# Kernel tuning notes

Measured on AMD Instinct MI355X. Metric: run time of the kernel, lower is better.

## Reference

```python
import jax, jax.numpy as jnp
import numpy as np

D_MODEL = 1024
NUM_HEADS = 16
D_K = D_MODEL // NUM_HEADS          # 64
D_ROPE = int(D_K * 0.5)             # 32
ROPE_BASE = 10000.0


def _rope(x):
    # x: [L, B, H, D_K]; rotate first D_ROPE features, pass the rest through.
    L = x.shape[0]
    d = D_ROPE
    theta = 1.0 / (ROPE_BASE ** (jnp.arange(0, d, 2, dtype=jnp.float32) / d))  # [d/2]
    idx_theta = jnp.arange(L, dtype=jnp.float32)[:, None] * theta[None, :]     # [L, d/2]
    idx_theta2 = jnp.concatenate([idx_theta, idx_theta], axis=-1)              # [L, d]
    cos = jnp.cos(idx_theta2)[:, None, None, :].astype(x.dtype)
    sin = jnp.sin(idx_theta2)[:, None, None, :].astype(x.dtype)
    x_rope, x_pass = x[..., :d], x[..., d:]
    neg_half = jnp.concatenate([-x_rope[..., d // 2:], x_rope[..., :d // 2]], axis=-1)
    x_rope = x_rope * cos + neg_half * sin
    return jnp.concatenate([x_rope, x_pass], axis=-1)


def setup_inputs() -> dict:
    key = jax.random.key(0)
    k1, k2 = jax.random.split(key)
    L, B = 2048, 2
    x = jax.random.normal(k1, (L, B, D_MODEL), dtype=jnp.float32)
    # xavier_uniform-like init for in_proj_weight [3*d_model, d_model]
    limit = float(np.sqrt(6.0 / (3 * D_MODEL + D_MODEL)))
    in_proj_weight = jax.random.uniform(k2, (3 * D_MODEL, D_MODEL),
                                        minval=-limit, maxval=limit, dtype=jnp.float32)
    return {"x": x, "in_proj_weight": in_proj_weight}


def reference(x, in_proj_weight):
    L, B, _ = x.shape
    # fused QKV projection: [L, B, 3*d_model]
    qkv = jnp.einsum('ed,lbd->lbe', in_proj_weight, x)
    # NOTE: faithful to original quirk — reshape to per-head blocks of 3*d_k,
    # then chunk along last dim.
    qkv = qkv.reshape(L, B, NUM_HEADS, 3 * D_K)
    q, k, v = qkv[..., :D_K], qkv[..., D_K:2 * D_K], qkv[..., 2 * D_K:]
    q = _rope(q)
    k = _rope(k)
    # [L,B,H,dk] -> [H,B,L,dk]
    q, k, v = (jnp.swapaxes(t, 0, 2) for t in (q, k, v))
    scale = 1.0 / jnp.sqrt(jnp.asarray(D_K, dtype=x.dtype))
    scores = jnp.einsum('hbqd,hbkd->hbqk', q, k) * scale      # [H,B,L,L]
    attn = jax.nn.softmax(scores, axis=-1)
    out = jnp.einsum('hbqk,hbkd->hbqd', attn, v)              # [H,B,L,dk]
    out = jnp.transpose(out, (1, 2, 0, 3)).reshape(B, L, D_MODEL)
    return jnp.swapaxes(out, 0, 1)                            # [L,B,D] (batch_first falsy)
```

## Files before the change

### kernel.cpp

```cpp
#include <hip/hip_runtime.h>
#include <cstdint>
#include <cstddef>

#define L_SEQ 2048
#define BATCH 2
#define DM 1024
#define NH 16
#define DK 64
#define QKV_N 3072
#define HEAD_STRIDE 192
#define NX (4096 * 1024)
#define NW (3072 * 1024)

typedef short short8_t __attribute__((ext_vector_type(8)));
typedef short short4_t __attribute__((ext_vector_type(4)));
typedef float f32x4 __attribute__((ext_vector_type(4)));

#define MFMA16(a, b, c) __builtin_amdgcn_mfma_f32_16x16x32_bf16(a, b, c, 0, 0, 0)

static __device__ __forceinline__ short f2b(float f) {
  union { float f; unsigned u; } v; v.f = f;
  unsigned r = v.u + 0x7FFFu + ((v.u >> 16) & 1u);
  return (short)(r >> 16);
}

static __device__ __forceinline__ void async_copy16(const unsigned short* g,
                                                    unsigned short* l) {
  __builtin_amdgcn_global_load_lds(
      (const __attribute__((address_space(1))) unsigned int*)g,
      (__attribute__((address_space(3))) unsigned int*)l, 16, 0, 0);
}

__global__ __launch_bounds__(256) void cast_kernel(
    const float* __restrict__ X, const float* __restrict__ W,
    unsigned short* __restrict__ dst) {
  const int e = (blockIdx.x * 256 + threadIdx.x) * 8;
  const float* src = (e < NX) ? &X[e] : &W[e - NX];
  const float4 v0 = *(const float4*)src;
  const float4 v1 = *(const float4*)(src + 4);
  short8_t s;
  s[0] = f2b(v0.x); s[1] = f2b(v0.y); s[2] = f2b(v0.z); s[3] = f2b(v0.w);
  s[4] = f2b(v1.x); s[5] = f2b(v1.y); s[6] = f2b(v1.z); s[7] = f2b(v1.w);
  *(short8_t*)&dst[e] = s;
}

__global__ __launch_bounds__(256) void qkv_gemm_bf16(
    const unsigned short* __restrict__ Xb, const unsigned short* __restrict__ Wb,
    unsigned short* __restrict__ qkvb) {
  __shared__ __align__(16) unsigned short As[128 * 32];
  __shared__ __align__(16) unsigned short Bs[128 * 32];
  const int t = threadIdx.x;
  const int w = t >> 6;
  const int lane = t & 63;
  const int L16 = lane & 15;
  const int quad = lane >> 4;
  const int m0 = blockIdx.y * 128;
  const int n0 = blockIdx.x * 128;
  const int wm = w & 1;
  const int wn = w >> 1;

  const int c0 = w * 128 + lane;
  const int c1 = c0 + 64;
  const unsigned short* gA0 = Xb + (size_t)(m0 + (c0 >> 2)) * 1024 + (c0 & 3) * 8;
  const unsigned short* gA1 = Xb + (size_t)(m0 + (c1 >> 2)) * 1024 + (c1 & 3) * 8;
  const unsigned short* gB0 = Wb + (size_t)(n0 + (c0 >> 2)) * 1024 + (c0 & 3) * 8;
  const unsigned short* gB1 = Wb + (size_t)(n0 + (c1 >> 2)) * 1024 + (c1 & 3) * 8;
  unsigned short* lA0 = &As[(w * 128) * 8];
  unsigned short* lA1 = &As[(w * 128 + 64) * 8];
  unsigned short* lB0 = &Bs[(w * 128) * 8];
  unsigned short* lB1 = &Bs[(w * 128 + 64) * 8];

  f32x4 acc[4][4];
#pragma unroll
  for (int i = 0; i < 4; ++i)
#pragma unroll
    for (int j = 0; j < 4; ++j) acc[i][j] = (f32x4){0.f, 0.f, 0.f, 0.f};

  for (int k0 = 0; k0 < 1024; k0 += 32) {
    async_copy16(gA0 + k0, lA0);
    async_copy16(gA1 + k0, lA1);
    async_copy16(gB0 + k0, lB0);
    async_copy16(gB1 + k0, lB1);
    __syncthreads();

    short8_t af[4], bfr[4];
#pragma unroll
    for (int mt = 0; mt < 4; ++mt)
      af[mt] = *(const short8_t*)&As[(wm * 64 + mt * 16 + L16) * 32 + quad * 8];
#pragma unroll
    for (int nt = 0; nt < 4; ++nt)
      bfr[nt] = *(const short8_t*)&Bs[(wn * 64 + nt * 16 + L16) * 32 + quad * 8];
#pragma unroll
    for (int mt = 0; mt < 4; ++mt)
#pragma unroll
      for (int nt = 0; nt < 4; ++nt)
        acc[mt][nt] = MFMA16(af[mt], bfr[nt], acc[mt][nt]);
    __syncthreads();
  }

  const int nbase = n0 + wn * 64 + L16;
  const int chunk = (n0 >> 6) + wn;
  const int type = chunk % 3;
  if (type == 2) {
#pragma unroll
    for (int mt = 0; mt < 4; ++mt) {
      const int mbase = m0 + wm * 64 + mt * 16 + quad * 4;
#pragma unroll
      for (int reg = 0; reg < 4; ++reg) {
        const size_t r = (size_t)(mbase + reg) * QKV_N + nbase;
        qkvb[r]      = (unsigned short)f2b(acc[mt][0][reg]);
        qkvb[r + 16] = (unsigned short)f2b(acc[mt][1][reg]);
        qkvb[r + 32] = (unsigned short)f2b(acc[mt][2][reg]);
        qkvb[r + 48] = (unsigned short)f2b(acc[mt][3][reg]);
      }
    }
  } else {
    const float qs = (type == 0) ? 0.125f : 1.0f;
    const float theta = exp2f(-(float)L16 * 0.8304820237218405f);
#pragma unroll
    for (int mt = 0; mt < 4; ++mt) {
      const int mbase = m0 + wm * 64 + mt * 16 + quad * 4;
      const int lb = mbase >> 1;
      float sv[2], cv[2];
      sincosf((float)lb * theta, &sv[0], &cv[0]);
      sincosf((float)(lb + 1) * theta, &sv[1], &cv[1]);
#pragma unroll
      for (int reg = 0; reg < 4; ++reg) {
        const int li = reg >> 1;
        const float v0 = acc[mt][0][reg], v1 = acc[mt][1][reg];
        const float r0 = v0 * cv[li] - v1 * sv[li];
        const float r1 = v1 * cv[li] + v0 * sv[li];
        const size_t r = (size_t)(mbase + reg) * QKV_N + nbase;
        qkvb[r]      = (unsigned short)f2b(r0 * qs);
        qkvb[r + 16] = (unsigned short)f2b(r1 * qs);
        qkvb[r + 32] = (unsigned short)f2b(acc[mt][2][reg] * qs);
        qkvb[r + 48] = (unsigned short)f2b(acc[mt][3][reg] * qs);
      }
    }
  }
}

__global__ __launch_bounds__(256) void attn_mfma_kernel(
    const unsigned short* __restrict__ qkvb, float* __restrict__ out) {
  __shared__ __align__(16) unsigned short Qs[128][72];
  __shared__ __align__(16) unsigned short Ks[64][72];
  __shared__ __align__(16) unsigned short Vt[64][72];
  __shared__ __align__(16) unsigned short Pw[4][32][72];

  const int t = threadIdx.x;
  const int w = t >> 6;
  const int lane = t & 63;
  const int L16 = lane & 15;
  const int quad = lane >> 4;
  const int l0 = blockIdx.x * 128;
  const int b = blockIdx.y & 1;
  const int h = blockIdx.y >> 1;
  const int hoff = h * HEAD_STRIDE;

#pragma unroll
  for (int it = 0; it < 4; ++it) {
    const int c = t + 256 * it;
    const int row = c >> 3;
    const int col = (c & 7) * 8;
    *(short8_t*)&Qs[row][col] =
        *(const short8_t*)&qkvb[((size_t)((l0 + row) * 2 + b)) * QKV_N + hoff + col];
  }
  __syncthreads();

  const short8_t aq00 = *(const short8_t*)&Qs[w * 32 + L16][quad * 8];
  const short8_t aq01 = *(const short8_t*)&Qs[w * 32 + L16][32 + quad * 8];
  const short8_t aq10 = *(const short8_t*)&Qs[w * 32 + 16 + L16][quad * 8];
  const short8_t aq11 = *(const short8_t*)&Qs[w * 32 + 16 + L16][32 + quad * 8];

  f32x4 oc[2][4];
  float l_part[2][4];
#pragma unroll
  for (int mt = 0; mt < 2; ++mt)
#pragma unroll
    for (int r = 0; r < 4; ++r) {
      l_part[mt][r] = 0.f;
      oc[mt][r] = (f32x4){0.f, 0.f, 0.f, 0.f};
    }

  const int krow0 = t >> 3, kcol0 = (t & 7) * 8;
  const int krow1 = (t + 256) >> 3, kcol1 = (t & 7) * 8;
  const int vr4 = (t >> 4) * 4;
  const int vc4 = (t & 15) * 4;
  const int cgbase = vr4 >> 3;
  const int joff = vr4 & 7;
  short8_t rk0, rk1;
  short4_t rv[4];

#define LOAD_TILE(KT)                                                         \
  {                                                                           \
    const int j0 = (KT) * 64;                                                 \
    rk0 = *(const short8_t*)&qkvb[((size_t)((j0 + krow0) * 2 + b)) * QKV_N +  \
                                  hoff + 64 + kcol0];                         \
    rk1 = *(const short8_t*)&qkvb[((size_t)((j0 + krow1) * 2 + b)) * QKV_N +  \
                                  hoff + 64 + kcol1];                         \
    _Pragma("unroll") for (int r = 0; r < 4; ++r)                             \
        rv[r] = *(const short4_t*)&qkvb[((size_t)((j0 + vr4 + r) * 2 + b)) *  \
                                        QKV_N + hoff + 128 + vc4];            \
  }

  LOAD_TILE(0)

  for (int kt = 0; kt < 32; ++kt) {
    __syncthreads();
    *(short8_t*)&Ks[krow0][kcol0] = rk0;
    *(short8_t*)&Ks[krow1][kcol1] = rk1;
    {
      short4_t s[4];
      s[0] = (short4_t){rv[0][0], rv[1][0], rv[2][0], rv[3][0]};
      s[1] = (short4_t){rv[0][1], rv[1][1], rv[2][1], rv[3][1]};
      s[2] = (short4_t){rv[0][2], rv[1][2], rv[2][2], rv[3][2]};
      s[3] = (short4_t){rv[0][3], rv[1][3], rv[2][3], rv[3][3]};
#pragma unroll
      for (int i = 0; i < 4; ++i) {
        const int d = vc4 + i;
        const int cg = (cgbase + ((d >> 2) & 7)) & 7;
        *(short4_t*)&Vt[d][cg * 8 + joff] = s[i];
      }
    }
    if (kt + 1 < 32) LOAD_TILE(kt + 1)
    __syncthreads();

    f32x4 sc[2][4];
#pragma unroll
    for (int mt = 0; mt < 2; ++mt)
#pragma unroll
      for (int nt = 0; nt < 4; ++nt) sc[mt][nt] = (f32x4){0.f, 0.f, 0.f, 0.f};
#pragma unroll
    for (int nt = 0; nt < 4; ++nt) {
      const short8_t b0 = *(const short8_t*)&Ks[nt * 16 + L16][quad * 8];
      const short8_t b1 = *(const short8_t*)&Ks[nt * 16 + L16][32 + quad * 8];
      sc[0][nt] = MFMA16(aq00, b0, sc[0][nt]);
      sc[0][nt] = MFMA16(aq01, b1, sc[0][nt]);
      sc[1][nt] = MFMA16(aq10, b0, sc[1][nt]);
      sc[1][nt] = MFMA16(aq11, b1, sc[1][nt]);
    }

#pragma unroll
    for (int mt = 0; mt < 2; ++mt) {
#pragma unroll
      for (int reg = 0; reg < 4; ++reg) {
        const int prow = mt * 16 + quad * 4 + reg;
#pragma unroll
        for (int nt = 0; nt < 4; ++nt) {
          const float p = __expf(sc[mt][nt][reg]);
          l_part[mt][reg] += p;
          Pw[w][prow][nt * 16 + L16] = (unsigned short)f2b(p);
        }
      }
    }

    const short8_t ap00 = *(const short8_t*)&Pw[w][L16][quad * 8];
    const short8_t ap01 = *(const short8_t*)&Pw[w][L16][32 + quad * 8];
    const short8_t ap10 = *(const short8_t*)&Pw[w][16 + L16][quad * 8];
    const short8_t ap11 = *(const short8_t*)&Pw[w][16 + L16][32 + quad * 8];
#pragma unroll
    for (int dt = 0; dt < 4; ++dt) {
      const int d = dt * 16 + L16;
      const int sh = (d >> 2) & 7;
      const short8_t bv0 = *(const short8_t*)&Vt[d][((quad + sh) & 7) * 8];
      const short8_t bv1 = *(const short8_t*)&Vt[d][((quad + 4 + sh) & 7) * 8];
      oc[0][dt] = MFMA16(ap00, bv0, oc[0][dt]);
      oc[0][dt] = MFMA16(ap01, bv1, oc[0][dt]);
      oc[1][dt] = MFMA16(ap10, bv0, oc[1][dt]);
      oc[1][dt] = MFMA16(ap11, bv1, oc[1][dt]);
    }
  }

#pragma unroll
  for (int mt = 0; mt < 2; ++mt) {
#pragma unroll
    for (int reg = 0; reg < 4; ++reg) {
      float l = l_part[mt][reg];
      l += __shfl_xor(l, 1);
      l += __shfl_xor(l, 2);
      l += __shfl_xor(l, 4);
      l += __shfl_xor(l, 8);
      const float inv = 1.f / l;
      const int qrow = l0 + w * 32 + mt * 16 + quad * 4 + reg;
      const size_t rbase = ((size_t)(qrow * 2 + b)) * DM + h * DK + L16;
#pragma unroll
      for (int dt = 0; dt < 4; ++dt) {
        out[rbase + dt * 16] = oc[mt][dt][reg] * inv;
      }
    }
  }
}

extern "C" void kernel_launch(void* const* d_in, const int* in_sizes, int n_in,
                              void* d_out, int out_size, void* d_ws,
                              size_t ws_size, hipStream_t stream) {
  const float* x = (const float*)d_in[0];
  const float* w = (const float*)d_in[1];
  float* out = (float*)d_out;
  unsigned short* bf = (unsigned short*)d_ws;
  unsigned short* Xb = bf;
  unsigned short* Wb = bf + NX;
  unsigned short* qkvb =
      (unsigned short*)((char*)d_ws + (16u << 20));

  cast_kernel<<<(NX + NW) / (256 * 8), 256, 0, stream>>>(x, w, bf);
  qkv_gemm_bf16<<<dim3(QKV_N / 128, (L_SEQ * BATCH) / 128), 256, 0, stream>>>(
      Xb, Wb, qkvb);
  attn_mfma_kernel<<<dim3(L_SEQ / 128, NH * BATCH), 256, 0, stream>>>(qkvb, out);
}
```

Baseline: 193.8 us.

## Compute transposed scores so P stays in registers, drop K/Q/P LDS staging

The attention kernel now computes S^T (K as the A operand, Q as B), so each lane's accumulator holds four consecutive keys for one query. Those probabilities can feed a 16x16x16 bf16 MFMA directly as the B operand, which removes the per-warp P round trip through LDS. Q and K fragments are loaded straight from global memory into registers instead of being staged in shared memory. V is double-buffered in LDS so one barrier per tile suffices, the output is written with float4 stores, and occupancy is hinted via launch bounds. The cost is more global K traffic, since each warp reloads K rather than sharing it, and twice as many smaller MFMA instructions for the PV product.

```diff
diff --git a/kernel.cpp b/kernel.cpp
--- a/kernel.cpp
+++ b/kernel.cpp
@@ -16,7 +16,8 @@
 typedef short short4_t __attribute__((ext_vector_type(4)));
 typedef float f32x4 __attribute__((ext_vector_type(4)));
 
-#define MFMA16(a, b, c) __builtin_amdgcn_mfma_f32_16x16x32_bf16(a, b, c, 0, 0, 0)
+#define MFMA32(a, b, c) __builtin_amdgcn_mfma_f32_16x16x32_bf16(a, b, c, 0, 0, 0)
+#define MFMA16(a, b, c) __builtin_amdgcn_mfma_f32_16x16x16bf16_1k(a, b, c, 0, 0, 0)
 
 static __device__ __forceinline__ short f2b(float f) {
   union { float f; unsigned u; } v; v.f = f;
@@ -94,7 +95,7 @@
     for (int mt = 0; mt < 4; ++mt)
 #pragma unroll
       for (int nt = 0; nt < 4; ++nt)
-        acc[mt][nt] = MFMA16(af[mt], bfr[nt], acc[mt][nt]);
+        acc[mt][nt] = MFMA32(af[mt], bfr[nt], acc[mt][nt]);
     __syncthreads();
   }
 
@@ -140,12 +141,9 @@
   }
 }
 
-__global__ __launch_bounds__(256) void attn_mfma_kernel(
+__global__ __launch_bounds__(256, 4) void attn_mfma_kernel(
     const unsigned short* __restrict__ qkvb, float* __restrict__ out) {
-  __shared__ __align__(16) unsigned short Qs[128][72];
-  __shared__ __align__(16) unsigned short Ks[64][72];
-  __shared__ __align__(16) unsigned short Vt[64][72];
-  __shared__ __align__(16) unsigned short Pw[4][32][72];
+  __shared__ __align__(16) unsigned short Vt[2][64][72];
 
   const int t = threadIdx.x;
   const int w = t >> 6;
@@ -157,58 +155,40 @@
   const int h = blockIdx.y >> 1;
   const int hoff = h * HEAD_STRIDE;
 
-#pragma unroll
-  for (int it = 0; it < 4; ++it) {
-    const int c = t + 256 * it;
-    const int row = c >> 3;
-    const int col = (c & 7) * 8;
-    *(short8_t*)&Qs[row][col] =
-        *(const short8_t*)&qkvb[((size_t)((l0 + row) * 2 + b)) * QKV_N + hoff + col];
-  }
-  __syncthreads();
-
-  const short8_t aq00 = *(const short8_t*)&Qs[w * 32 + L16][quad * 8];
-  const short8_t aq01 = *(const short8_t*)&Qs[w * 32 + L16][32 + quad * 8];
-  const short8_t aq10 = *(const short8_t*)&Qs[w * 32 + 16 + L16][quad * 8];
-  const short8_t aq11 = *(const short8_t*)&Qs[w * 32 + 16 + L16][32 + quad * 8];
+  short8_t bq[2][2];
+#pragma unroll
+  for (int mt = 0; mt < 2; ++mt)
+#pragma unroll
+    for (int kc = 0; kc < 2; ++kc)
+      bq[mt][kc] = *(const short8_t*)
+          &qkvb[((size_t)((l0 + w * 32 + mt * 16 + L16) * 2 + b)) * QKV_N +
+                hoff + kc * 32 + quad * 8];
 
   f32x4 oc[2][4];
-  float l_part[2][4];
+  float l_part[2] = {0.f, 0.f};
 #pragma unroll
   for (int mt = 0; mt < 2; ++mt)
 #pragma unroll
-    for (int r = 0; r < 4; ++r) {
-      l_part[mt][r] = 0.f;
-      oc[mt][r] = (f32x4){0.f, 0.f, 0.f, 0.f};
-    }
-
-  const int krow0 = t >> 3, kcol0 = (t & 7) * 8;
-  const int krow1 = (t + 256) >> 3, kcol1 = (t & 7) * 8;
+    for (int dt = 0; dt < 4; ++dt) oc[mt][dt] = (f32x4){0.f, 0.f, 0.f, 0.f};
+
   const int vr4 = (t >> 4) * 4;
   const int vc4 = (t & 15) * 4;
   const int cgbase = vr4 >> 3;
   const int joff = vr4 & 7;
-  short8_t rk0, rk1;
   short4_t rv[4];
 
-#define LOAD_TILE(KT)                                                         \
+#define LOAD_V(KT)                                                            \
   {                                                                           \
     const int j0 = (KT) * 64;                                                 \
-    rk0 = *(const short8_t*)&qkvb[((size_t)((j0 + krow0) * 2 + b)) * QKV_N +  \
-                                  hoff + 64 + kcol0];                         \
-    rk1 = *(const short8_t*)&qkvb[((size_t)((j0 + krow1) * 2 + b)) * QKV_N +  \
-                                  hoff + 64 + kcol1];                         \
     _Pragma("unroll") for (int r = 0; r < 4; ++r)                             \
         rv[r] = *(const short4_t*)&qkvb[((size_t)((j0 + vr4 + r) * 2 + b)) *  \
                                         QKV_N + hoff + 128 + vc4];            \
   }
 
-  LOAD_TILE(0)
+  LOAD_V(0)
 
   for (int kt = 0; kt < 32; ++kt) {
-    __syncthreads();
-    *(short8_t*)&Ks[krow0][kcol0] = rk0;
-    *(short8_t*)&Ks[krow1][kcol1] = rk1;
+    const int buf = kt & 1;
     {
       short4_t s[4];
       s[0] = (short4_t){rv[0][0], rv[1][0], rv[2][0], rv[3][0]};
@@ -219,12 +199,14 @@
       for (int i = 0; i < 4; ++i) {
         const int d = vc4 + i;
         const int cg = (cgbase + ((d >> 2) & 7)) & 7;
-        *(short4_t*)&Vt[d][cg * 8 + joff] = s[i];
-      }
-    }
-    if (kt + 1 < 32) LOAD_TILE(kt + 1)
+        *(short4_t*)&Vt[buf][d][cg * 8 + joff] = s[i];
+      }
+    }
+    if (kt + 1 < 32) LOAD_V(kt + 1)
     __syncthreads();
 
+    const int j0 = kt * 64;
+
     f32x4 sc[2][4];
 #pragma unroll
     for (int mt = 0; mt < 2; ++mt)
@@ -232,61 +214,56 @@
       for (int nt = 0; nt < 4; ++nt) sc[mt][nt] = (f32x4){0.f, 0.f, 0.f, 0.f};
 #pragma unroll
     for (int nt = 0; nt < 4; ++nt) {
-      const short8_t b0 = *(const short8_t*)&Ks[nt * 16 + L16][quad * 8];
-      const short8_t b1 = *(const short8_t*)&Ks[nt * 16 + L16][32 + quad * 8];
-      sc[0][nt] = MFMA16(aq00, b0, sc[0][nt]);
-      sc[0][nt] = MFMA16(aq01, b1, sc[0][nt]);
-      sc[1][nt] = MFMA16(aq10, b0, sc[1][nt]);
-      sc[1][nt] = MFMA16(aq11, b1, sc[1][nt]);
-    }
-
+      const size_t krow = (size_t)((j0 + nt * 16 + L16) * 2 + b) * QKV_N + hoff + 64;
+      const short8_t ak0 = *(const short8_t*)&qkvb[krow + quad * 8];
+      const short8_t ak1 = *(const short8_t*)&qkvb[krow + 32 + quad * 8];
+      sc[0][nt] = MFMA32(ak0, bq[0][0], sc[0][nt]);
+      sc[0][nt] = MFMA32(ak1, bq[0][1], sc[0][nt]);
+      sc[1][nt] = MFMA32(ak0, bq[1][0], sc[1][nt]);
+      sc[1][nt] = MFMA32(ak1, bq[1][1], sc[1][nt]);
+    }
+
+    short4_t pf[2][4];
 #pragma unroll
     for (int mt = 0; mt < 2; ++mt) {
 #pragma unroll
-      for (int reg = 0; reg < 4; ++reg) {
-        const int prow = mt * 16 + quad * 4 + reg;
-#pragma unroll
-        for (int nt = 0; nt < 4; ++nt) {
-          const float p = __expf(sc[mt][nt][reg]);
-          l_part[mt][reg] += p;
-          Pw[w][prow][nt * 16 + L16] = (unsigned short)f2b(p);
-        }
-      }
-    }
-
-    const short8_t ap00 = *(const short8_t*)&Pw[w][L16][quad * 8];
-    const short8_t ap01 = *(const short8_t*)&Pw[w][L16][32 + quad * 8];
-    const short8_t ap10 = *(const short8_t*)&Pw[w][16 + L16][quad * 8];
-    const short8_t ap11 = *(const short8_t*)&Pw[w][16 + L16][32 + quad * 8];
+      for (int nt = 0; nt < 4; ++nt) {
+        float p0 = __expf(sc[mt][nt][0]);
+        float p1 = __expf(sc[mt][nt][1]);
+        float p2 = __expf(sc[mt][nt][2]);
+        float p3 = __expf(sc[mt][nt][3]);
+        l_part[mt] += (p0 + p1) + (p2 + p3);
+        pf[mt][nt] = (short4_t){f2b(p0), f2b(p1), f2b(p2), f2b(p3)};
+      }
+    }
+
+#pragma unroll
+    for (int nt = 0; nt < 4; ++nt) {
+#pragma unroll
+      for (int dt = 0; dt < 4; ++dt) {
+        const int d = dt * 16 + L16;
+        const int g = 2 * nt + (quad >> 1);
+        const int cg = (g + ((d >> 2) & 7)) & 7;
+        const short4_t vf = *(const short4_t*)&Vt[buf][d][cg * 8 + (quad & 1) * 4];
+        oc[0][dt] = MFMA16(vf, pf[0][nt], oc[0][dt]);
+        oc[1][dt] = MFMA16(vf, pf[1][nt], oc[1][dt]);
+      }
+    }
+  }
+
+#pragma unroll
+  for (int mt = 0; mt < 2; ++mt) {
+    float l = l_part[mt];
+    l += __shfl_xor(l, 16);
+    l += __shfl_xor(l, 32);
+    const float inv = 1.f / l;
+    const int qrow = l0 + w * 32 + mt * 16 + L16;
+    const size_t rbase = ((size_t)(qrow * 2 + b)) * DM + h * DK;
 #pragma unroll
     for (int dt = 0; dt < 4; ++dt) {
-      const int d = dt * 16 + L16;
-      const int sh = (d >> 2) & 7;
-      const short8_t bv0 = *(const short8_t*)&Vt[d][((quad + sh) & 7) * 8];
-      const short8_t bv1 = *(const short8_t*)&Vt[d][((quad + 4 + sh) & 7) * 8];
-      oc[0][dt] = MFMA16(ap00, bv0, oc[0][dt]);
-      oc[0][dt] = MFMA16(ap01, bv1, oc[0][dt]);
-      oc[1][dt] = MFMA16(ap10, bv0, oc[1][dt]);
-      oc[1][dt] = MFMA16(ap11, bv1, oc[1][dt]);
-    }
-  }
-
-#pragma unroll
-  for (int mt = 0; mt < 2; ++mt) {
-#pragma unroll
-    for (int reg = 0; reg < 4; ++reg) {
-      float l = l_part[mt][reg];
-      l += __shfl_xor(l, 1);
-      l += __shfl_xor(l, 2);
-      l += __shfl_xor(l, 4);
-      l += __shfl_xor(l, 8);
-      const float inv = 1.f / l;
-      const int qrow = l0 + w * 32 + mt * 16 + quad * 4 + reg;
-      const size_t rbase = ((size_t)(qrow * 2 + b)) * DM + h * DK + L16;
-#pragma unroll
-      for (int dt = 0; dt < 4; ++dt) {
-        out[rbase + dt * 16] = oc[mt][dt][reg] * inv;
-      }
+      *(float4*)&out[rbase + dt * 16 + quad * 4] =
+          make_float4(oc[mt][dt][0] * inv, oc[mt][dt][1] * inv,
+                      oc[mt][dt][2] * inv, oc[mt][dt][3] * inv);
     }
   }
 }
```

Result: slower. 266.5 us (+37.5%).
